# Performance work log

Hardware: AMD Instinct MI355X
Metric: run time of the kernel (lower is better)

## Reference

```python
import jax, jax.numpy as jnp
import numpy as np

RHO = 1.0
EPSILON = 0.1
N_ITERS = 5
EPS = 1e-08


def setup_inputs() -> dict:
    key = jax.random.key(0)
    k1, k2, k3 = jax.random.split(key, 3)
    B, H, M, N, D = 16, 16, 256, 576, 1024
    # student cross-attention weights: positive, rows roughly sum to 1 (post-softmax in the real model)
    sa = jax.random.uniform(k1, (B, H, M, N), dtype=jnp.float32) + 1e-3
    student_attn = sa / sa.sum(axis=-1, keepdims=True)
    visual_feats = jax.random.normal(k2, (B, N, D), dtype=jnp.float32)
    text_feats = jax.random.normal(k3, (B, M, D), dtype=jnp.float32)
    text_mask = jnp.ones((B, M), dtype=jnp.float32)
    return {"student_attn": student_attn, "visual_feats": visual_feats,
            "text_feats": text_feats, "text_mask": text_mask}


def _l2norm(x):
    return x / jnp.sqrt(jnp.sum(x * x, axis=-1, keepdims=True) + 1e-12)


def _teacher_plan(x, y, y_mask):
    # x: (B,N,D) visual, y: (B,M,D) text, y_mask: (B,M)
    B, N, D = x.shape
    M = y.shape[1]
    x_n = _l2norm(x)
    y_n = _l2norm(y)
    cost = 1.0 - jnp.einsum('bmd,bnd->bmn', y_n, x_n)          # (B,M,N)
    mu = jnp.full((B, N, 1), 1.0 / N, dtype=x.dtype)            # visual marginal (column vec)
    nu = (y_mask / (jnp.sum(y_mask, axis=1, keepdims=True) + EPS))[:, :, None]  # (B,M,1)
    K = jnp.exp(-cost / EPSILON)                                # (B,M,N)
    fi = RHO / (RHO + EPSILON)
    u = jnp.ones((B, M, 1), dtype=x.dtype)
    v = jnp.ones((B, N, 1), dtype=x.dtype)
    for _ in range(N_ITERS):
        Kv = jnp.einsum('bmn,bnk->bmk', K, v)                   # (B,M,1)
        u = (nu / (Kv + EPS)) ** fi
        Ktu = jnp.einsum('bmn,bmk->bnk', K, u)                  # (B,N,1)
        v = (mu / (Ktu + EPS)) ** fi
    P = u * K * jnp.swapaxes(v, 1, 2)                           # (B,M,N)
    return P / (jnp.sum(P, axis=-1, keepdims=True) + EPS)


def reference(student_attn, visual_feats, text_feats, text_mask):
    teacher = jax.lax.stop_gradient(_teacher_plan(visual_feats, text_feats, text_mask))
    teacher = teacher[:, None, :, :]                            # (B,1,M,N)
    loss = -jnp.sum(teacher * jnp.log(student_attn + EPS), axis=-1)  # (B,H,M)
    loss = loss * text_mask[:, None, :]
    return jnp.mean(loss)
```

## Files before the change

kernel.cpp:

```cpp
#include <hip/hip_runtime.h>
#include <math.h>

#define B_ 16
#define H_ 16
#define M_ 256
#define N_ 576
#define D_ 1024
#define BK 64
#define LDS_STRIDE (BK + 8)
#define NROWS (B_ * N_ + B_ * M_)

#define SINK_BLOCKS B_
#define SUMLOG_BLOCKS ((B_ * M_ * N_ / 4) / 1024)

constexpr float EPS_ = 1e-8f;
constexpr float FI_ = 0.90909090909090906f;

typedef __bf16 bf16x8 __attribute__((ext_vector_type(8)));
typedef float f32x4 __attribute__((ext_vector_type(4)));

__device__ __forceinline__ float wave_reduce(float v) {
#pragma unroll
  for (int o = 32; o > 0; o >>= 1) v += __shfl_down(v, o, 64);
  return v;
}

__device__ __forceinline__ unsigned short f2bf(float f) {
  union { float f; unsigned u; } a; a.f = f;
  unsigned r = a.u + 0x7fff + ((a.u >> 16) & 1);
  return (unsigned short)(r >> 16);
}

__device__ __forceinline__ float bf2f(unsigned short u) {
  union { unsigned u; float f; } a; a.u = ((unsigned)u) << 16;
  return a.f;
}

__global__ __launch_bounds__(256) void prep_kernel(const float* __restrict__ vis,
                                                   const float* __restrict__ txt,
                                                   const float* __restrict__ mask,
                                                   unsigned short* __restrict__ xb,
                                                   unsigned short* __restrict__ yb,
                                                   float* __restrict__ masksum) {
  const int bid = blockIdx.x;
  const int lane = threadIdx.x & 63;
  if (bid < NROWS / 4) {
    int wave = bid * 4 + (threadIdx.x >> 6);
    const float* src;
    unsigned short* dst;
    if (wave < B_ * N_) {
      src = vis + (size_t)wave * D_;
      dst = xb + (size_t)wave * D_;
    } else {
      int r = wave - B_ * N_;
      src = txt + (size_t)r * D_;
      dst = yb + (size_t)r * D_;
    }
    float4 v[4];
    float s = 0.f;
#pragma unroll
    for (int it = 0; it < 4; ++it) {
      v[it] = *(const float4*)&src[it * 256 + lane * 4];
      s += v[it].x * v[it].x + v[it].y * v[it].y + v[it].z * v[it].z + v[it].w * v[it].w;
    }
    s = wave_reduce(s);
    s = __shfl(s, 0, 64);
    float inv = rsqrtf(s + 1e-12f);
#pragma unroll
    for (int it = 0; it < 4; ++it) {
      ushort4 pk;
      pk.x = f2bf(v[it].x * inv);
      pk.y = f2bf(v[it].y * inv);
      pk.z = f2bf(v[it].z * inv);
      pk.w = f2bf(v[it].w * inv);
      *(ushort4*)&dst[it * 256 + lane * 4] = pk;
    }
  } else {
    int b = (bid - NROWS / 4) * 4 + (threadIdx.x >> 6);
    float4 mv = *(const float4*)&mask[b * M_ + lane * 4];
    float s = wave_reduce(mv.x + mv.y + mv.z + mv.w);
    if (lane == 0) masksum[b] = s;
  }
}

__global__ __launch_bounds__(256) void gemm_k_mfma(const unsigned short* __restrict__ xb,
                                                   const unsigned short* __restrict__ yb,
                                                   unsigned short* __restrict__ Kw) {
  __shared__ unsigned short As[64][LDS_STRIDE];
  __shared__ unsigned short Bs[64][LDS_STRIDE];
  const int b = blockIdx.z;
  const int m0 = blockIdx.y * 64;
  const int n0 = blockIdx.x * 64;
  const unsigned short* Y = yb + (size_t)b * M_ * D_;
  const unsigned short* X = xb + (size_t)b * N_ * D_;
  const int t = threadIdx.x;
  const int lane = t & 63;
  const int w = t >> 6;
  const int wm = (w & 1) * 32;
  const int wn = (w >> 1) * 32;
  const int lr = t >> 3;
  const int lc = (t & 7) * 8;
  const int fr = lane & 15;
  const int fk = (lane >> 4) * 8;

  f32x4 acc[2][2] = {};
  for (int k0 = 0; k0 < D_; k0 += BK) {
#pragma unroll
    for (int p = 0; p < 2; ++p) {
      *(uint4*)&As[lr + 32 * p][lc] = *(const uint4*)&Y[(size_t)(m0 + lr + 32 * p) * D_ + k0 + lc];
      *(uint4*)&Bs[lr + 32 * p][lc] = *(const uint4*)&X[(size_t)(n0 + lr + 32 * p) * D_ + k0 + lc];
    }
    __syncthreads();
#pragma unroll
    for (int ks = 0; ks < BK; ks += 32) {
      bf16x8 a[2], bfr[2];
#pragma unroll
      for (int i = 0; i < 2; ++i) {
        a[i] = *(const bf16x8*)&As[wm + i * 16 + fr][ks + fk];
        bfr[i] = *(const bf16x8*)&Bs[wn + i * 16 + fr][ks + fk];
      }
#pragma unroll
      for (int i = 0; i < 2; ++i)
#pragma unroll
        for (int j = 0; j < 2; ++j)
          acc[i][j] = __builtin_amdgcn_mfma_f32_16x16x32_bf16(a[i], bfr[j], acc[i][j], 0, 0, 0);
    }
    __syncthreads();
  }

  const int cm = (lane >> 4) * 4;
  const int cn = lane & 15;
#pragma unroll
  for (int i = 0; i < 2; ++i)
#pragma unroll
    for (int j = 0; j < 2; ++j)
#pragma unroll
      for (int rg = 0; rg < 4; ++rg) {
        int m = m0 + wm + i * 16 + cm + rg;
        int n = n0 + wn + j * 16 + cn;
        Kw[((size_t)b * M_ + m) * N_ + n] = f2bf(expf(10.f * (acc[i][j][rg] - 1.f)));
      }
}

__global__ __launch_bounds__(1024) void sink_sumlog_kernel(
    const unsigned short* __restrict__ Kw,
    const float* __restrict__ mask,
    const float* __restrict__ masksum,
    const float* __restrict__ student,
    float* __restrict__ SL,
    float* __restrict__ vv) {
  if (blockIdx.x >= SINK_BLOCKS) {
    const int t = threadIdx.x;
    const int idx = (blockIdx.x - SINK_BLOCKS) * 1024 + t;
    const int b = idx / (M_ * N_ / 4);
    const int cb = idx - b * (M_ * N_ / 4);
    const float* st = student + (size_t)b * H_ * M_ * N_ + (size_t)cb * 4;
    float4 acc = {0.f, 0.f, 0.f, 0.f};
#pragma unroll
    for (int h = 0; h < H_; ++h) {
      float4 s4 = *(const float4*)&st[(size_t)h * M_ * N_];
      acc.x += __logf(s4.x + EPS_);
      acc.y += __logf(s4.y + EPS_);
      acc.z += __logf(s4.z + EPS_);
      acc.w += __logf(s4.w + EPS_);
    }
    *(float4*)&SL[(size_t)b * M_ * N_ + (size_t)cb * 4] = acc;
    return;
  }

  __shared__ float u_s[M_];
  __shared__ float v_s[N_];
  __shared__ float nu_s[M_];
  __shared__ float vp[4][N_];
  const int b = blockIdx.x;
  const int t = threadIdx.x;
  const int lane = t & 63;
  const int w = t >> 6;
  const unsigned short* Kb = Kw + (size_t)b * M_ * N_;

  if (t < M_) nu_s[t] = mask[b * M_ + t] / (masksum[b] + EPS_);
  if (t < N_) v_s[t] = 1.f;
  __syncthreads();

  for (int it = 0; it < 5; ++it) {
#pragma unroll 2
    for (int r = 0; r < 16; ++r) {
      const int m = w * 16 + r;
      const unsigned short* rp = Kb + (size_t)m * N_;
      float s = 0.f;
#pragma unroll
      for (int k = 0; k < 9; ++k) s += bf2f(rp[lane + 64 * k]) * v_s[lane + 64 * k];
      s = wave_reduce(s);
      if (lane == 0) u_s[m] = powf(nu_s[m] / (s + EPS_), FI_);
    }
    __syncthreads();

    if (t < 576) {
      const int q = t / 144;
      const int c4 = (t - q * 144) * 4;
      float s0 = 0.f, s1 = 0.f, s2 = 0.f, s3 = 0.f;
#pragma unroll 8
      for (int m = q * 64; m < q * 64 + 64; ++m) {
        ushort4 k4 = *(const ushort4*)&Kb[(size_t)m * N_ + c4];
        const float um = u_s[m];
        s0 += bf2f(k4.x) * um;
        s1 += bf2f(k4.y) * um;
        s2 += bf2f(k4.z) * um;
        s3 += bf2f(k4.w) * um;
      }
      float4 r4 = {s0, s1, s2, s3};
      *(float4*)&vp[q][c4] = r4;
    }
    __syncthreads();
    if (t < N_) {
      float tot = vp[0][t] + vp[1][t] + vp[2][t] + vp[3][t];
      v_s[t] = powf((1.f / (float)N_) / (tot + EPS_), FI_);
    }
    __syncthreads();
  }
  if (t < N_) vv[b * N_ + t] = v_s[t];
}

__global__ __launch_bounds__(256) void finloss_kernel(const unsigned short* __restrict__ Kw,
                                                      const float* __restrict__ SL,
                                                      const float* __restrict__ v,
                                                      const float* __restrict__ mask,
                                                      float* __restrict__ partial) {
  __shared__ float red[2][4];
  const int m = blockIdx.x;
  const int b = blockIdx.y;
  const int t = threadIdx.x;
  float s1 = 0.f, s2 = 0.f;
  if (t < N_ / 4) {
    const unsigned short* kp = Kw + ((size_t)b * M_ + m) * N_ + t * 4;
    ushort4 k4 = *(const ushort4*)kp;
    float4 v4 = *(const float4*)&v[b * N_ + t * 4];
    float4 sl4 = *(const float4*)&SL[((size_t)b * M_ + m) * N_ + t * 4];
    float kv0 = bf2f(k4.x) * v4.x, kv1 = bf2f(k4.y) * v4.y;
    float kv2 = bf2f(k4.z) * v4.z, kv3 = bf2f(k4.w) * v4.w;
    s1 = kv0 + kv1 + kv2 + kv3;
    s2 = kv0 * sl4.x + kv1 * sl4.y + kv2 * sl4.z + kv3 * sl4.w;
  }
  s1 = wave_reduce(s1);
  s2 = wave_reduce(s2);
  if ((t & 63) == 0) { red[0][t >> 6] = s1; red[1][t >> 6] = s2; }
  __syncthreads();
  if (t == 0) {
    float S1 = red[0][0] + red[0][1] + red[0][2] + red[0][3];
    float S2 = red[1][0] + red[1][1] + red[1][2] + red[1][3];
    int row = b * M_ + m;
    partial[row] = -mask[row] * S2 / ((S1 + EPS_) * (float)(B_ * H_ * M_));
  }
}

__global__ __launch_bounds__(256) void reduce_kernel(const float* __restrict__ partial,
                                                     float* __restrict__ out) {
  __shared__ float red[4];
  float s = 0.f;
  for (int i = threadIdx.x; i < B_ * M_; i += 256) s += partial[i];
  s = wave_reduce(s);
  if ((threadIdx.x & 63) == 0) red[threadIdx.x >> 6] = s;
  __syncthreads();
  if (threadIdx.x == 0) out[0] = red[0] + red[1] + red[2] + red[3];
}

extern "C" void kernel_launch(void* const* d_in, const int* in_sizes, int n_in,
                              void* d_out, int out_size, void* d_ws, size_t ws_size,
                              hipStream_t stream) {
  const float* student = (const float*)d_in[0];
  const float* vis = (const float*)d_in[1];
  const float* txt = (const float*)d_in[2];
  const float* mask = (const float*)d_in[3];
  float* out = (float*)d_out;

  char* p = (char*)d_ws;
  unsigned short* Kb = (unsigned short*)p; p += (size_t)B_ * M_ * N_ * 2;
  unsigned short* xb = (unsigned short*)p; p += (size_t)B_ * N_ * D_ * 2;
  unsigned short* yb = (unsigned short*)p; p += (size_t)B_ * M_ * D_ * 2;
  float* SL = (float*)p;      p += (size_t)B_ * M_ * N_ * 4;
  float* vv = (float*)p;      p += B_ * N_ * 4;
  float* msum = (float*)p;    p += B_ * 4;
  float* partial = (float*)p; p += B_ * M_ * 4;

  prep_kernel<<<NROWS / 4 + 4, 256, 0, stream>>>(vis, txt, mask, xb, yb, msum);
  gemm_k_mfma<<<dim3(N_ / 64, M_ / 64, B_), 256, 0, stream>>>(xb, yb, Kb);

  sink_sumlog_kernel<<<SINK_BLOCKS + SUMLOG_BLOCKS, 1024, 0, stream>>>(
      Kb, mask, msum, student, SL, vv);

  finloss_kernel<<<dim3(M_, B_), 256, 0, stream>>>(Kb, SL, vv, mask, partial);
  reduce_kernel<<<1, 256, 0, stream>>>(partial, out);
}
```

Baseline: 399.0 us.

## Cache bf16 kernel matrix in registers across Sinkhorn iterations

Each wave loads its 16 rows of the bf16 K matrix into packed registers once, before the Sinkhorn loop. Both the row pass (K·v) and the column pass (Kᵀ·u) then run from those registers, so K is no longer re-read from global memory in each of the five iterations. The column pass now accumulates per-wave partial sums into the shared vp array in four serialized phases, separated by barriers. This raises register pressure and adds barriers in exchange for removing repeated memory traffic in a kernel that runs on only 16 blocks.

Measured after the change: 403.9 us. No clear change (+1.2%).

```diff
diff --git a/kernel.cpp b/kernel.cpp
--- a/kernel.cpp
+++ b/kernel.cpp
@@ -34,6 +34,13 @@
 __device__ __forceinline__ float bf2f(unsigned short u) {
   union { unsigned u; float f; } a; a.u = ((unsigned)u) << 16;
   return a.f;
+}
+
+__device__ __forceinline__ float bflo(unsigned p) {
+  union { unsigned u; float f; } a; a.u = p << 16; return a.f;
+}
+__device__ __forceinline__ float bfhi(unsigned p) {
+  union { unsigned u; float f; } a; a.u = p & 0xffff0000u; return a.f;
 }
 
 __global__ __launch_bounds__(256) void prep_kernel(const float* __restrict__ vis,
@@ -171,6 +178,7 @@
   __shared__ float u_s[M_];
   __shared__ float v_s[N_];
   __shared__ float nu_s[M_];
+  __shared__ float sred[M_];
   __shared__ float vp[4][N_];
   const int b = blockIdx.x;
   const int t = threadIdx.x;
@@ -178,42 +186,68 @@
   const int w = t >> 6;
   const unsigned short* Kb = Kw + (size_t)b * M_ * N_;
 
+  unsigned kp[16][4];
+  unsigned k8[8];
+#pragma unroll
+  for (int r = 0; r < 16; ++r) {
+    const unsigned short* rp = Kb + (size_t)((w << 4) + r) * N_ + lane;
+#pragma unroll
+    for (int j = 0; j < 4; ++j)
+      kp[r][j] = (unsigned)rp[128 * j] | ((unsigned)rp[128 * j + 64] << 16);
+    unsigned t8 = rp[512];
+    if (r & 1) k8[r >> 1] |= t8 << 16; else k8[r >> 1] = t8;
+  }
+
   if (t < M_) nu_s[t] = mask[b * M_ + t] / (masksum[b] + EPS_);
   if (t < N_) v_s[t] = 1.f;
   __syncthreads();
 
   for (int it = 0; it < 5; ++it) {
-#pragma unroll 2
+    float vl[9];
+#pragma unroll
+    for (int k = 0; k < 9; ++k) vl[k] = v_s[lane + 64 * k];
+
+#pragma unroll
     for (int r = 0; r < 16; ++r) {
-      const int m = w * 16 + r;
-      const unsigned short* rp = Kb + (size_t)m * N_;
       float s = 0.f;
 #pragma unroll
-      for (int k = 0; k < 9; ++k) s += bf2f(rp[lane + 64 * k]) * v_s[lane + 64 * k];
+      for (int j = 0; j < 4; ++j) {
+        s += bflo(kp[r][j]) * vl[2 * j];
+        s += bfhi(kp[r][j]) * vl[2 * j + 1];
+      }
+      s += ((r & 1) ? bfhi(k8[r >> 1]) : bflo(k8[r >> 1])) * vl[8];
       s = wave_reduce(s);
-      if (lane == 0) u_s[m] = powf(nu_s[m] / (s + EPS_), FI_);
-    }
-    __syncthreads();
-
-    if (t < 576) {
-      const int q = t / 144;
-      const int c4 = (t - q * 144) * 4;
-      float s0 = 0.f, s1 = 0.f, s2 = 0.f, s3 = 0.f;
-#pragma unroll 8
-      for (int m = q * 64; m < q * 64 + 64; ++m) {
-        ushort4 k4 = *(const ushort4*)&Kb[(size_t)m * N_ + c4];
-        const float um = u_s[m];
-        s0 += bf2f(k4.x) * um;
-        s1 += bf2f(k4.y) * um;
-        s2 += bf2f(k4.z) * um;
-        s3 += bf2f(k4.w) * um;
+      if (lane == 0) sred[(w << 4) + r] = s;
+    }
+    if (lane < 16) {
+      const int m = (w << 4) + lane;
+      u_s[m] = powf(nu_s[m] / (sred[m] + EPS_), FI_);
+    }
+
+#pragma unroll
+    for (int s = 0; s < 4; ++s) {
+      if ((w & 3) == s) {
+        const int q = w >> 2;
+        float uw[16];
+#pragma unroll
+        for (int r = 0; r < 16; ++r) uw[r] = u_s[(w << 4) + r];
+#pragma unroll
+        for (int k = 0; k < 9; ++k) {
+          float tmp = (s == 0) ? 0.f : vp[q][lane + 64 * k];
+#pragma unroll
+          for (int r = 0; r < 16; ++r) {
+            float kv;
+            if (k < 8) kv = (k & 1) ? bfhi(kp[r][k >> 1]) : bflo(kp[r][k >> 1]);
+            else       kv = (r & 1) ? bfhi(k8[r >> 1]) : bflo(k8[r >> 1]);
+            tmp += kv * uw[r];
+          }
+          vp[q][lane + 64 * k] = tmp;
+        }
       }
-      float4 r4 = {s0, s1, s2, s3};
-      *(float4*)&vp[q][c4] = r4;
-    }
-    __syncthreads();
+      __syncthreads();
+    }
     if (t < N_) {
-      float tot = vp[0][t] + vp[1][t] + vp[2][t] + vp[3][t];
+      float tot = ((vp[0][t] + vp[1][t]) + vp[2][t]) + vp[3][t];
       v_s[t] = powf((1.f / (float)N_) / (tot + EPS_), FI_);
     }
     __syncthreads();
```

## Fuse all stages into one cooperative persistent kernel with grid-wide phase syncs

Applied to the files above, without the earlier changes.

Replaces the five separate kernels with a single cooperative mega-kernel that runs prep, GEMM, ten Sinkhorn half-steps, the final loss and the reduction as phases separated by grid syncs. The Sinkhorn solve is now spread across all blocks instead of one block per batch. The student log-sum work is split into ten slices and interleaved with the Sinkhorn phases to fill idle CUs. This trades launch overhead and the serialized per-batch Sinkhorn for the cost of many grid-wide barriers and a smaller GEMM tile per block. A per-phase launch path is kept as a fallback if cooperative launch fails.

New measurement: 770.7 us. +93.2%, slower.

```diff
diff --git a/kernel.cpp b/kernel.cpp
--- a/kernel.cpp
+++ b/kernel.cpp
@@ -1,17 +1,18 @@
 #include <hip/hip_runtime.h>
+#include <hip/hip_cooperative_groups.h>
 #include <math.h>
+
+namespace cg = cooperative_groups;
 
 #define B_ 16
 #define H_ 16
 #define M_ 256
 #define N_ 576
 #define D_ 1024
-#define BK 64
-#define LDS_STRIDE (BK + 8)
 #define NROWS (B_ * N_ + B_ * M_)
-
-#define SINK_BLOCKS B_
-#define SUMLOG_BLOCKS ((B_ * M_ * N_ / 4) / 1024)
+#define SL_UNITS (B_ * M_ * N_ / 4)
+#define GEMM_TILES (B_ * (M_ / 64) * (N_ / 64))
+#define NPHASE 14
 
 constexpr float EPS_ = 1e-8f;
 constexpr float FI_ = 0.90909090909090906f;
@@ -36,232 +37,220 @@
   return a.f;
 }
 
-__global__ __launch_bounds__(256) void prep_kernel(const float* __restrict__ vis,
-                                                   const float* __restrict__ txt,
-                                                   const float* __restrict__ mask,
-                                                   unsigned short* __restrict__ xb,
-                                                   unsigned short* __restrict__ yb,
-                                                   float* __restrict__ masksum) {
+__global__ __launch_bounds__(512, 4) void mega_kernel(
+    const float* __restrict__ student, const float* __restrict__ vis,
+    const float* __restrict__ txt, const float* __restrict__ mask,
+    unsigned short* __restrict__ xb, unsigned short* __restrict__ yb,
+    unsigned short* __restrict__ Kw, float* __restrict__ SL,
+    float* __restrict__ uu, float* __restrict__ vv,
+    float* __restrict__ msum, float* __restrict__ partial,
+    float* __restrict__ out, int plo, int phi) {
+  __shared__ unsigned short As[64][72];
+  __shared__ unsigned short Bs[64][72];
+  __shared__ float part[4][64];
+  __shared__ float redf[2][2][4];
+  __shared__ float redr[4];
+
+  const int tid = threadIdx.x;
+  const int lane = tid & 63;
+  const int w = tid >> 6;
   const int bid = blockIdx.x;
-  const int lane = threadIdx.x & 63;
-  if (bid < NROWS / 4) {
-    int wave = bid * 4 + (threadIdx.x >> 6);
-    const float* src;
-    unsigned short* dst;
-    if (wave < B_ * N_) {
-      src = vis + (size_t)wave * D_;
-      dst = xb + (size_t)wave * D_;
+  const int GRID = gridDim.x;
+
+  for (int ph = plo; ph < phi; ++ph) {
+    if (ph > plo) cg::this_grid().sync();
+
+    if (ph == 0) {
+      for (int row = bid * 8 + w; row < NROWS + B_; row += GRID * 8) {
+        if (row < NROWS) {
+          const float* src;
+          unsigned short* dst;
+          if (row < B_ * N_) {
+            src = vis + (size_t)row * D_;
+            dst = xb + (size_t)row * D_;
+          } else {
+            int r = row - B_ * N_;
+            src = txt + (size_t)r * D_;
+            dst = yb + (size_t)r * D_;
+          }
+          float4 v[4];
+          float s = 0.f;
+#pragma unroll
+          for (int it = 0; it < 4; ++it) {
+            v[it] = *(const float4*)&src[it * 256 + lane * 4];
+            s += v[it].x * v[it].x + v[it].y * v[it].y + v[it].z * v[it].z + v[it].w * v[it].w;
+          }
+          s = wave_reduce(s);
+          s = __shfl(s, 0, 64);
+          float inv = rsqrtf(s + 1e-12f);
+#pragma unroll
+          for (int it = 0; it < 4; ++it) {
+            ushort4 pk;
+            pk.x = f2bf(v[it].x * inv);
+            pk.y = f2bf(v[it].y * inv);
+            pk.z = f2bf(v[it].z * inv);
+            pk.w = f2bf(v[it].w * inv);
+            *(ushort4*)&dst[it * 256 + lane * 4] = pk;
+          }
+        } else {
+          int b = row - NROWS;
+          float4 mv = *(const float4*)&mask[b * M_ + lane * 4];
+          float s = wave_reduce(mv.x + mv.y + mv.z + mv.w);
+          if (lane == 0) msum[b] = s;
+        }
+      }
+
+    } else if (ph == 1) {
+      const int lr = tid >> 3;
+      const int lc = (tid & 7) * 8;
+      const int am = (w & 3) * 16;
+      const int wn = (w >> 2) * 32;
+      const int fr = lane & 15;
+      const int fk = (lane >> 4) * 8;
+      const int cm = (lane >> 4) * 4;
+      const int cn = lane & 15;
+      for (int tt = bid; tt < GEMM_TILES; tt += GRID) {
+        const int b = tt / 36;
+        const int rem = tt - b * 36;
+        const int m0 = (rem / 9) * 64;
+        const int n0 = (rem - (rem / 9) * 9) * 64;
+        const unsigned short* Y = yb + (size_t)b * M_ * D_;
+        const unsigned short* X = xb + (size_t)b * N_ * D_;
+        f32x4 acc[2] = {};
+        for (int k0 = 0; k0 < D_; k0 += 64) {
+          __syncthreads();
+          *(uint4*)&As[lr][lc] = *(const uint4*)&Y[(size_t)(m0 + lr) * D_ + k0 + lc];
+          *(uint4*)&Bs[lr][lc] = *(const uint4*)&X[(size_t)(n0 + lr) * D_ + k0 + lc];
+          __syncthreads();
+#pragma unroll
+          for (int ks = 0; ks < 64; ks += 32) {
+            bf16x8 a = *(const bf16x8*)&As[am + fr][ks + fk];
+            bf16x8 b0 = *(const bf16x8*)&Bs[wn + fr][ks + fk];
+            bf16x8 b1 = *(const bf16x8*)&Bs[wn + 16 + fr][ks + fk];
+            acc[0] = __builtin_amdgcn_mfma_f32_16x16x32_bf16(a, b0, acc[0], 0, 0, 0);
+            acc[1] = __builtin_amdgcn_mfma_f32_16x16x32_bf16(a, b1, acc[1], 0, 0, 0);
+          }
+        }
+#pragma unroll
+        for (int j = 0; j < 2; ++j)
+#pragma unroll
+          for (int rg = 0; rg < 4; ++rg) {
+            int m = m0 + am + cm + rg;
+            int n = n0 + wn + j * 16 + cn;
+            Kw[((size_t)b * M_ + m) * N_ + n] = f2bf(expf(10.f * (acc[j][rg] - 1.f)));
+          }
+      }
+
+    } else if (ph < 12) {
+      const int sp = ph - 2;
+      if ((sp & 1) == 0) {
+        for (int row = bid * 8 + w; row < B_ * M_; row += GRID * 8) {
+          const unsigned short* rp = Kw + (size_t)row * N_;
+          float s = 0.f;
+          if (sp == 0) {
+#pragma unroll
+            for (int k = 0; k < 9; ++k) s += bf2f(rp[lane + 64 * k]);
+          } else {
+            const float* vb = vv + (row >> 8) * N_;
+#pragma unroll
+            for (int k = 0; k < 9; ++k) s += bf2f(rp[lane + 64 * k]) * vb[lane + 64 * k];
+          }
+          s = wave_reduce(s);
+          if (lane == 0) {
+            float nu = mask[row] / (msum[row >> 8] + EPS_);
+            uu[row] = powf(nu / (s + EPS_), FI_);
+          }
+        }
+      } else {
+        for (int unit = bid; unit < B_ * (N_ / 64); unit += GRID) {
+          const int b = unit / 9;
+          const int n0 = (unit - b * 9) * 64;
+          const unsigned short* Kb2 = Kw + (size_t)b * M_ * N_;
+          const float* ub = uu + b * M_;
+          if (w < 4) {
+            const int col = n0 + lane;
+            float s = 0.f;
+#pragma unroll 8
+            for (int m = w * 64; m < (w + 1) * 64; ++m)
+              s += bf2f(Kb2[(size_t)m * N_ + col]) * ub[m];
+            part[w][lane] = s;
+          }
+          __syncthreads();
+          if (tid < 64) {
+            float tot = part[0][tid] + part[1][tid] + part[2][tid] + part[3][tid];
+            vv[b * N_ + n0 + tid] = powf((1.f / (float)N_) / (tot + EPS_), FI_);
+          }
+          __syncthreads();
+        }
+      }
+      {
+        const int c0 = (int)(((long long)SL_UNITS * sp) / 10);
+        const int c1 = (int)(((long long)SL_UNITS * (sp + 1)) / 10);
+        const int nblk = (c1 - c0 + 511) >> 9;
+        const int rb = (bid + (sp * GRID) / 10) % GRID;
+        if (rb < nblk) {
+          const int u = c0 + (rb << 9) + tid;
+          if (u < c1) {
+            const int b = u / (M_ * N_ / 4);
+            const int cb = u - b * (M_ * N_ / 4);
+            const float* st = student + (size_t)b * H_ * M_ * N_ + (size_t)cb * 4;
+            float4 acc = {0.f, 0.f, 0.f, 0.f};
+#pragma unroll
+            for (int h = 0; h < H_; ++h) {
+              float4 s4 = *(const float4*)&st[(size_t)h * M_ * N_];
+              acc.x += __logf(s4.x + EPS_);
+              acc.y += __logf(s4.y + EPS_);
+              acc.z += __logf(s4.z + EPS_);
+              acc.w += __logf(s4.w + EPS_);
+            }
+            *(float4*)&SL[(size_t)b * M_ * N_ + (size_t)cb * 4] = acc;
+          }
+        }
+      }
+
+    } else if (ph == 12) {
+      const int half = tid >> 8;
+      const int lt = tid & 255;
+      const int stride = GRID * 2;
+      const int cnt = (B_ * M_ - 1 - bid * 2) / stride + 1;
+      for (int i = 0; i < cnt; ++i) {
+        const int unit = bid * 2 + half + i * stride;
+        float s1 = 0.f, s2 = 0.f;
+        if (unit < B_ * M_ && lt < 144) {
+          const int b = unit >> 8;
+          const unsigned short* kp = Kw + (size_t)unit * N_ + lt * 4;
+          ushort4 k4 = *(const ushort4*)kp;
+          float4 v4 = *(const float4*)&vv[b * N_ + lt * 4];
+          float4 sl4 = *(const float4*)&SL[(size_t)unit * N_ + lt * 4];
+          float kv0 = bf2f(k4.x) * v4.x, kv1 = bf2f(k4.y) * v4.y;
+          float kv2 = bf2f(k4.z) * v4.z, kv3 = bf2f(k4.w) * v4.w;
+          s1 = kv0 + kv1 + kv2 + kv3;
+          s2 = kv0 * sl4.x + kv1 * sl4.y + kv2 * sl4.z + kv3 * sl4.w;
+        }
+        s1 = wave_reduce(s1);
+        s2 = wave_reduce(s2);
+        if ((lt & 63) == 0) { redf[half][0][lt >> 6] = s1; redf[half][1][lt >> 6] = s2; }
+        __syncthreads();
+        if (lt == 0 && unit < B_ * M_) {
+          float S1 = redf[half][0][0] + redf[half][0][1] + redf[half][0][2] + redf[half][0][3];
+          float S2 = redf[half][1][0] + redf[half][1][1] + redf[half][1][2] + redf[half][1][3];
+          partial[unit] = -mask[unit] * S2 / ((S1 + EPS_) * (float)(B_ * H_ * M_));
+        }
+        __syncthreads();
+      }
+
     } else {
-      int r = wave - B_ * N_;
-      src = txt + (size_t)r * D_;
-      dst = yb + (size_t)r * D_;
+      if (bid == 0) {
+        float s = 0.f;
+        if (tid < 256)
+          for (int i = tid; i < B_ * M_; i += 256) s += partial[i];
+        s = wave_reduce(s);
+        if (tid < 256 && (tid & 63) == 0) redr[tid >> 6] = s;
+        __syncthreads();
+        if (tid == 0) out[0] = redr[0] + redr[1] + redr[2] + redr[3];
+      }
     }
-    float4 v[4];
-    float s = 0.f;
-#pragma unroll
-    for (int it = 0; it < 4; ++it) {
-      v[it] = *(const float4*)&src[it * 256 + lane * 4];
-      s += v[it].x * v[it].x + v[it].y * v[it].y + v[it].z * v[it].z + v[it].w * v[it].w;
-    }
-    s = wave_reduce(s);
-    s = __shfl(s, 0, 64);
-    float inv = rsqrtf(s + 1e-12f);
-#pragma unroll
-    for (int it = 0; it < 4; ++it) {
-      ushort4 pk;
-      pk.x = f2bf(v[it].x * inv);
-      pk.y = f2bf(v[it].y * inv);
-      pk.z = f2bf(v[it].z * inv);
-      pk.w = f2bf(v[it].w * inv);
-      *(ushort4*)&dst[it * 256 + lane * 4] = pk;
-    }
-  } else {
-    int b = (bid - NROWS / 4) * 4 + (threadIdx.x >> 6);
-    float4 mv = *(const float4*)&mask[b * M_ + lane * 4];
-    float s = wave_reduce(mv.x + mv.y + mv.z + mv.w);
-    if (lane == 0) masksum[b] = s;
   }
-}
-
-__global__ __launch_bounds__(256) void gemm_k_mfma(const unsigned short* __restrict__ xb,
-                                                   const unsigned short* __restrict__ yb,
-                                                   unsigned short* __restrict__ Kw) {
-  __shared__ unsigned short As[64][LDS_STRIDE];
-  __shared__ unsigned short Bs[64][LDS_STRIDE];
-  const int b = blockIdx.z;
-  const int m0 = blockIdx.y * 64;
-  const int n0 = blockIdx.x * 64;
-  const unsigned short* Y = yb + (size_t)b * M_ * D_;
-  const unsigned short* X = xb + (size_t)b * N_ * D_;
-  const int t = threadIdx.x;
-  const int lane = t & 63;
-  const int w = t >> 6;
-  const int wm = (w & 1) * 32;
-  const int wn = (w >> 1) * 32;
-  const int lr = t >> 3;
-  const int lc = (t & 7) * 8;
-  const int fr = lane & 15;
-  const int fk = (lane >> 4) * 8;
-
-  f32x4 acc[2][2] = {};
-  for (int k0 = 0; k0 < D_; k0 += BK) {
-#pragma unroll
-    for (int p = 0; p < 2; ++p) {
-      *(uint4*)&As[lr + 32 * p][lc] = *(const uint4*)&Y[(size_t)(m0 + lr + 32 * p) * D_ + k0 + lc];
-      *(uint4*)&Bs[lr + 32 * p][lc] = *(const uint4*)&X[(size_t)(n0 + lr + 32 * p) * D_ + k0 + lc];
-    }
-    __syncthreads();
-#pragma unroll
-    for (int ks = 0; ks < BK; ks += 32) {
-      bf16x8 a[2], bfr[2];
-#pragma unroll
-      for (int i = 0; i < 2; ++i) {
-        a[i] = *(const bf16x8*)&As[wm + i * 16 + fr][ks + fk];
-        bfr[i] = *(const bf16x8*)&Bs[wn + i * 16 + fr][ks + fk];
-      }
-#pragma unroll
-      for (int i = 0; i < 2; ++i)
-#pragma unroll
-        for (int j = 0; j < 2; ++j)
-          acc[i][j] = __builtin_amdgcn_mfma_f32_16x16x32_bf16(a[i], bfr[j], acc[i][j], 0, 0, 0);
-    }
-    __syncthreads();
-  }
-
-  const int cm = (lane >> 4) * 4;
-  const int cn = lane & 15;
-#pragma unroll
-  for (int i = 0; i < 2; ++i)
-#pragma unroll
-    for (int j = 0; j < 2; ++j)
-#pragma unroll
-      for (int rg = 0; rg < 4; ++rg) {
-        int m = m0 + wm + i * 16 + cm + rg;
-        int n = n0 + wn + j * 16 + cn;
-        Kw[((size_t)b * M_ + m) * N_ + n] = f2bf(expf(10.f * (acc[i][j][rg] - 1.f)));
-      }
-}
-
-__global__ __launch_bounds__(1024) void sink_sumlog_kernel(
-    const unsigned short* __restrict__ Kw,
-    const float* __restrict__ mask,
-    const float* __restrict__ masksum,
-    const float* __restrict__ student,
-    float* __restrict__ SL,
-    float* __restrict__ vv) {
-  if (blockIdx.x >= SINK_BLOCKS) {
-    const int t = threadIdx.x;
-    const int idx = (blockIdx.x - SINK_BLOCKS) * 1024 + t;
-    const int b = idx / (M_ * N_ / 4);
-    const int cb = idx - b * (M_ * N_ / 4);
-    const float* st = student + (size_t)b * H_ * M_ * N_ + (size_t)cb * 4;
-    float4 acc = {0.f, 0.f, 0.f, 0.f};
-#pragma unroll
-    for (int h = 0; h < H_; ++h) {
-      float4 s4 = *(const float4*)&st[(size_t)h * M_ * N_];
-      acc.x += __logf(s4.x + EPS_);
-      acc.y += __logf(s4.y + EPS_);
-      acc.z += __logf(s4.z + EPS_);
-      acc.w += __logf(s4.w + EPS_);
-    }
-    *(float4*)&SL[(size_t)b * M_ * N_ + (size_t)cb * 4] = acc;
-    return;
-  }
-
-  __shared__ float u_s[M_];
-  __shared__ float v_s[N_];
-  __shared__ float nu_s[M_];
-  __shared__ float vp[4][N_];
-  const int b = blockIdx.x;
-  const int t = threadIdx.x;
-  const int lane = t & 63;
-  const int w = t >> 6;
-  const unsigned short* Kb = Kw + (size_t)b * M_ * N_;
-
-  if (t < M_) nu_s[t] = mask[b * M_ + t] / (masksum[b] + EPS_);
-  if (t < N_) v_s[t] = 1.f;
-  __syncthreads();
-
-  for (int it = 0; it < 5; ++it) {
-#pragma unroll 2
-    for (int r = 0; r < 16; ++r) {
-      const int m = w * 16 + r;
-      const unsigned short* rp = Kb + (size_t)m * N_;
-      float s = 0.f;
-#pragma unroll
-      for (int k = 0; k < 9; ++k) s += bf2f(rp[lane + 64 * k]) * v_s[lane + 64 * k];
-      s = wave_reduce(s);
-      if (lane == 0) u_s[m] = powf(nu_s[m] / (s + EPS_), FI_);
-    }
-    __syncthreads();
-
-    if (t < 576) {
-      const int q = t / 144;
-      const int c4 = (t - q * 144) * 4;
-      float s0 = 0.f, s1 = 0.f, s2 = 0.f, s3 = 0.f;
-#pragma unroll 8
-      for (int m = q * 64; m < q * 64 + 64; ++m) {
-        ushort4 k4 = *(const ushort4*)&Kb[(size_t)m * N_ + c4];
-        const float um = u_s[m];
-        s0 += bf2f(k4.x) * um;
-        s1 += bf2f(k4.y) * um;
-        s2 += bf2f(k4.z) * um;
-        s3 += bf2f(k4.w) * um;
-      }
-      float4 r4 = {s0, s1, s2, s3};
-      *(float4*)&vp[q][c4] = r4;
-    }
-    __syncthreads();
-    if (t < N_) {
-      float tot = vp[0][t] + vp[1][t] + vp[2][t] + vp[3][t];
-      v_s[t] = powf((1.f / (float)N_) / (tot + EPS_), FI_);
-    }
-    __syncthreads();
-  }
-  if (t < N_) vv[b * N_ + t] = v_s[t];
-}
-
-__global__ __launch_bounds__(256) void finloss_kernel(const unsigned short* __restrict__ Kw,
-                                                      const float* __restrict__ SL,
-                                                      const float* __restrict__ v,
-                                                      const float* __restrict__ mask,
-                                                      float* __restrict__ partial) {
-  __shared__ float red[2][4];
-  const int m = blockIdx.x;
-  const int b = blockIdx.y;
-  const int t = threadIdx.x;
-  float s1 = 0.f, s2 = 0.f;
-  if (t < N_ / 4) {
-    const unsigned short* kp = Kw + ((size_t)b * M_ + m) * N_ + t * 4;
-    ushort4 k4 = *(const ushort4*)kp;
-    float4 v4 = *(const float4*)&v[b * N_ + t * 4];
-    float4 sl4 = *(const float4*)&SL[((size_t)b * M_ + m) * N_ + t * 4];
-    float kv0 = bf2f(k4.x) * v4.x, kv1 = bf2f(k4.y) * v4.y;
-    float kv2 = bf2f(k4.z) * v4.z, kv3 = bf2f(k4.w) * v4.w;
-    s1 = kv0 + kv1 + kv2 + kv3;
-    s2 = kv0 * sl4.x + kv1 * sl4.y + kv2 * sl4.z + kv3 * sl4.w;
-  }
-  s1 = wave_reduce(s1);
-  s2 = wave_reduce(s2);
-  if ((t & 63) == 0) { red[0][t >> 6] = s1; red[1][t >> 6] = s2; }
-  __syncthreads();
-  if (t == 0) {
-    float S1 = red[0][0] + red[0][1] + red[0][2] + red[0][3];
-    float S2 = red[1][0] + red[1][1] + red[1][2] + red[1][3];
-    int row = b * M_ + m;
-    partial[row] = -mask[row] * S2 / ((S1 + EPS_) * (float)(B_ * H_ * M_));
-  }
-}
-
-__global__ __launch_bounds__(256) void reduce_kernel(const float* __restrict__ partial,
-                                                     float* __restrict__ out) {
-  __shared__ float red[4];
-  float s = 0.f;
-  for (int i = threadIdx.x; i < B_ * M_; i += 256) s += partial[i];
-  s = wave_reduce(s);
-  if ((threadIdx.x & 63) == 0) red[threadIdx.x >> 6] = s;
-  __syncthreads();
-  if (threadIdx.x == 0) out[0] = red[0] + red[1] + red[2] + red[3];
 }
 
 extern "C" void kernel_launch(void* const* d_in, const int* in_sizes, int n_in,
@@ -274,20 +263,45 @@
   float* out = (float*)d_out;
 
   char* p = (char*)d_ws;
-  unsigned short* Kb = (unsigned short*)p; p += (size_t)B_ * M_ * N_ * 2;
+  unsigned short* Kw = (unsigned short*)p; p += (size_t)B_ * M_ * N_ * 2;
   unsigned short* xb = (unsigned short*)p; p += (size_t)B_ * N_ * D_ * 2;
   unsigned short* yb = (unsigned short*)p; p += (size_t)B_ * M_ * D_ * 2;
   float* SL = (float*)p;      p += (size_t)B_ * M_ * N_ * 4;
   float* vv = (float*)p;      p += B_ * N_ * 4;
+  float* uu = (float*)p;      p += B_ * M_ * 4;
   float* msum = (float*)p;    p += B_ * 4;
   float* partial = (float*)p; p += B_ * M_ * 4;
 
-  prep_kernel<<<NROWS / 4 + 4, 256, 0, stream>>>(vis, txt, mask, xb, yb, msum);
-  gemm_k_mfma<<<dim3(N_ / 64, M_ / 64, B_), 256, 0, stream>>>(xb, yb, Kb);
-
-  sink_sumlog_kernel<<<SINK_BLOCKS + SUMLOG_BLOCKS, 1024, 0, stream>>>(
-      Kb, mask, msum, student, SL, vv);
-
-  finloss_kernel<<<dim3(M_, B_), 256, 0, stream>>>(Kb, SL, vv, mask, partial);
-  reduce_kernel<<<1, 256, 0, stream>>>(partial, out);
-}
+  static int coop_blocks = -2;
+  if (coop_blocks == -2) {
+    int dev = 0;
+    (void)hipGetDevice(&dev);
+    int has_coop = 0;
+    (void)hipDeviceGetAttribute(&has_coop, hipDeviceAttributeCooperativeLaunch, dev);
+    int nb = 0;
+    hipError_t e = hipOccupancyMaxActiveBlocksPerMultiprocessor(
+        &nb, reinterpret_cast<const void*>(&mega_kernel), 512, 0);
+    coop_blocks = (has_coop && e == hipSuccess && nb >= 1) ? nb : 0;
+  }
+
+  bool launched = false;
+  if (coop_blocks > 0) {
+    int grid = coop_blocks * 256;
+    if (grid > 512) grid = 512;
+    int plo = 0, phi = NPHASE;
+    void* args[] = {(void*)&student, (void*)&vis,  (void*)&txt,  (void*)&mask,
+                    (void*)&xb,      (void*)&yb,   (void*)&Kw,   (void*)&SL,
+                    (void*)&uu,      (void*)&vv,   (void*)&msum, (void*)&partial,
+                    (void*)&out,     (void*)&plo,  (void*)&phi};
+    hipError_t e = hipLaunchCooperativeKernel(
+        reinterpret_cast<const void*>(&mega_kernel), dim3(grid), dim3(512),
+        args, 0, stream);
+    launched = (e == hipSuccess);
+  }
+  if (!launched) {
+    for (int ph2 = 0; ph2 < NPHASE; ++ph2)
+      mega_kernel<<<dim3(512), dim3(512), 0, stream>>>(
+          student, vis, txt, mask, xb, yb, Kw, SL, uu, vv, msum, partial, out,
+          ph2, ph2 + 1);
+  }
+}
```

## Split Sinkhorn across four blocks per batch with LDS slabs and fused finalization

Applied to the files above, without the earlier changes.

Moves the student log-sum pass into the GEMM launch so it runs alongside K generation. The Sinkhorn loop is split across four blocks per batch, each holding a 64-row slab of K in shared memory. Per-iteration column sums are combined through global buffers behind an atomic-counter barrier. The final loss and global reduction are folded into the same kernel with a last-block-done reduction, removing two launches. This trades the single 1024-thread block per batch and repeated global K reads for spin-wait inter-block sync, which assumes all 64 blocks are co-resident.

New measurement: 424.6 us. 1.06x slower.

```diff
diff --git a/kernel.cpp b/kernel.cpp
--- a/kernel.cpp
+++ b/kernel.cpp
@@ -9,9 +9,9 @@
 #define BK 64
 #define LDS_STRIDE (BK + 8)
 #define NROWS (B_ * N_ + B_ * M_)
-
-#define SINK_BLOCKS B_
-#define SUMLOG_BLOCKS ((B_ * M_ * N_ / 4) / 1024)
+#define SL_UNITS (B_ * M_ * N_ / 4)
+#define GEMM_BLOCKS (B_ * 4 * 9)
+#define SUMLOG_BLK (SL_UNITS / 256)
 
 constexpr float EPS_ = 1e-8f;
 constexpr float FI_ = 0.90909090909090906f;
@@ -41,7 +41,8 @@
                                                    const float* __restrict__ mask,
                                                    unsigned short* __restrict__ xb,
                                                    unsigned short* __restrict__ yb,
-                                                   float* __restrict__ masksum) {
+                                                   float* __restrict__ masksum,
+                                                   int* __restrict__ ctr) {
   const int bid = blockIdx.x;
   const int lane = threadIdx.x & 63;
   if (bid < NROWS / 4) {
@@ -76,6 +77,7 @@
       *(ushort4*)&dst[it * 256 + lane * 4] = pk;
     }
   } else {
+    if (bid == NROWS / 4 && threadIdx.x < 96) ctr[threadIdx.x] = 0;
     int b = (bid - NROWS / 4) * 4 + (threadIdx.x >> 6);
     float4 mv = *(const float4*)&mask[b * M_ + lane * 4];
     float s = wave_reduce(mv.x + mv.y + mv.z + mv.w);
@@ -83,14 +85,36 @@
   }
 }
 
-__global__ __launch_bounds__(256) void gemm_k_mfma(const unsigned short* __restrict__ xb,
-                                                   const unsigned short* __restrict__ yb,
-                                                   unsigned short* __restrict__ Kw) {
+__global__ __launch_bounds__(256) void gemm_sumlog_kernel(
+    const unsigned short* __restrict__ xb, const unsigned short* __restrict__ yb,
+    const float* __restrict__ student, unsigned short* __restrict__ Kw,
+    float* __restrict__ SL) {
   __shared__ unsigned short As[64][LDS_STRIDE];
   __shared__ unsigned short Bs[64][LDS_STRIDE];
-  const int b = blockIdx.z;
-  const int m0 = blockIdx.y * 64;
-  const int n0 = blockIdx.x * 64;
+
+  if (blockIdx.x >= GEMM_BLOCKS) {
+    const int unit = (blockIdx.x - GEMM_BLOCKS) * 256 + threadIdx.x;
+    const int b = unit / (M_ * N_ / 4);
+    const int cb = unit - b * (M_ * N_ / 4);
+    const float* st = student + (size_t)b * H_ * M_ * N_ + (size_t)cb * 4;
+    float4 acc = {0.f, 0.f, 0.f, 0.f};
+#pragma unroll
+    for (int h = 0; h < H_; ++h) {
+      float4 s4 = *(const float4*)&st[(size_t)h * M_ * N_];
+      acc.x += __logf(s4.x + EPS_);
+      acc.y += __logf(s4.y + EPS_);
+      acc.z += __logf(s4.z + EPS_);
+      acc.w += __logf(s4.w + EPS_);
+    }
+    *(float4*)&SL[(size_t)b * M_ * N_ + (size_t)cb * 4] = acc;
+    return;
+  }
+
+  const int tile = blockIdx.x;
+  const int b = tile / 36;
+  const int rem = tile - b * 36;
+  const int m0 = (rem / 9) * 64;
+  const int n0 = (rem - (rem / 9) * 9) * 64;
   const unsigned short* Y = yb + (size_t)b * M_ * D_;
   const unsigned short* X = xb + (size_t)b * N_ * D_;
   const int t = threadIdx.x;
@@ -142,126 +166,119 @@
       }
 }
 
-__global__ __launch_bounds__(1024) void sink_sumlog_kernel(
-    const unsigned short* __restrict__ Kw,
-    const float* __restrict__ mask,
-    const float* __restrict__ masksum,
-    const float* __restrict__ student,
-    float* __restrict__ SL,
-    float* __restrict__ vv) {
-  if (blockIdx.x >= SINK_BLOCKS) {
-    const int t = threadIdx.x;
-    const int idx = (blockIdx.x - SINK_BLOCKS) * 1024 + t;
-    const int b = idx / (M_ * N_ / 4);
-    const int cb = idx - b * (M_ * N_ / 4);
-    const float* st = student + (size_t)b * H_ * M_ * N_ + (size_t)cb * 4;
-    float4 acc = {0.f, 0.f, 0.f, 0.f};
-#pragma unroll
-    for (int h = 0; h < H_; ++h) {
-      float4 s4 = *(const float4*)&st[(size_t)h * M_ * N_];
-      acc.x += __logf(s4.x + EPS_);
-      acc.y += __logf(s4.y + EPS_);
-      acc.z += __logf(s4.z + EPS_);
-      acc.w += __logf(s4.w + EPS_);
-    }
-    *(float4*)&SL[(size_t)b * M_ * N_ + (size_t)cb * 4] = acc;
-    return;
-  }
-
-  __shared__ float u_s[M_];
+__global__ __launch_bounds__(256) void sink_fin_kernel(
+    const unsigned short* __restrict__ Kw, const float* __restrict__ SL,
+    const float* __restrict__ mask, const float* __restrict__ msum,
+    float* __restrict__ vp_g, int* __restrict__ ctr,
+    float* __restrict__ partial, float* __restrict__ out) {
+  __shared__ unsigned short slab[64][N_];
   __shared__ float v_s[N_];
-  __shared__ float nu_s[M_];
-  __shared__ float vp[4][N_];
-  const int b = blockIdx.x;
+  __shared__ float u_s[64];
+  __shared__ float nu_s[64];
+  __shared__ float red[2][4];
+  __shared__ float redr[4];
+  __shared__ int lastflag;
+
   const int t = threadIdx.x;
   const int lane = t & 63;
   const int w = t >> 6;
-  const unsigned short* Kb = Kw + (size_t)b * M_ * N_;
-
-  if (t < M_) nu_s[t] = mask[b * M_ + t] / (masksum[b] + EPS_);
-  if (t < N_) v_s[t] = 1.f;
+  const int b = blockIdx.x >> 2;
+  const int q = blockIdx.x & 3;
+  const int row0 = q * 64;
+
+  const unsigned short* Kbase = Kw + ((size_t)b * M_ + row0) * N_;
+  for (int i = t; i < 64 * 72; i += 256) {
+    const int r = i / 72;
+    const int c8 = (i - r * 72) * 8;
+    *(uint4*)&slab[r][c8] = *(const uint4*)&Kbase[(size_t)r * N_ + c8];
+  }
+  if (t < 64) nu_s[t] = mask[b * M_ + row0 + t] / (msum[b] + EPS_);
+  for (int n = t; n < N_; n += 256) v_s[n] = 1.f;
   __syncthreads();
+
+  float* vp_b = vp_g + (size_t)b * 2 * 4 * N_;
 
   for (int it = 0; it < 5; ++it) {
 #pragma unroll 2
     for (int r = 0; r < 16; ++r) {
       const int m = w * 16 + r;
-      const unsigned short* rp = Kb + (size_t)m * N_;
       float s = 0.f;
 #pragma unroll
-      for (int k = 0; k < 9; ++k) s += bf2f(rp[lane + 64 * k]) * v_s[lane + 64 * k];
+      for (int k = 0; k < 9; ++k) s += bf2f(slab[m][lane + 64 * k]) * v_s[lane + 64 * k];
       s = wave_reduce(s);
       if (lane == 0) u_s[m] = powf(nu_s[m] / (s + EPS_), FI_);
     }
     __syncthreads();
 
-    if (t < 576) {
-      const int q = t / 144;
-      const int c4 = (t - q * 144) * 4;
-      float s0 = 0.f, s1 = 0.f, s2 = 0.f, s3 = 0.f;
+    const int par = it & 1;
+    float* vp_out = vp_b + (size_t)(par * 4 + q) * N_;
+    for (int c = t; c < N_; c += 256) {
+      float s = 0.f;
 #pragma unroll 8
-      for (int m = q * 64; m < q * 64 + 64; ++m) {
-        ushort4 k4 = *(const ushort4*)&Kb[(size_t)m * N_ + c4];
-        const float um = u_s[m];
-        s0 += bf2f(k4.x) * um;
-        s1 += bf2f(k4.y) * um;
-        s2 += bf2f(k4.z) * um;
-        s3 += bf2f(k4.w) * um;
-      }
-      float4 r4 = {s0, s1, s2, s3};
-      *(float4*)&vp[q][c4] = r4;
-    }
-    __syncthreads();
-    if (t < N_) {
-      float tot = vp[0][t] + vp[1][t] + vp[2][t] + vp[3][t];
-      v_s[t] = powf((1.f / (float)N_) / (tot + EPS_), FI_);
-    }
-    __syncthreads();
-  }
-  if (t < N_) vv[b * N_ + t] = v_s[t];
-}
-
-__global__ __launch_bounds__(256) void finloss_kernel(const unsigned short* __restrict__ Kw,
-                                                      const float* __restrict__ SL,
-                                                      const float* __restrict__ v,
-                                                      const float* __restrict__ mask,
-                                                      float* __restrict__ partial) {
-  __shared__ float red[2][4];
-  const int m = blockIdx.x;
-  const int b = blockIdx.y;
-  const int t = threadIdx.x;
-  float s1 = 0.f, s2 = 0.f;
-  if (t < N_ / 4) {
-    const unsigned short* kp = Kw + ((size_t)b * M_ + m) * N_ + t * 4;
-    ushort4 k4 = *(const ushort4*)kp;
-    float4 v4 = *(const float4*)&v[b * N_ + t * 4];
-    float4 sl4 = *(const float4*)&SL[((size_t)b * M_ + m) * N_ + t * 4];
-    float kv0 = bf2f(k4.x) * v4.x, kv1 = bf2f(k4.y) * v4.y;
-    float kv2 = bf2f(k4.z) * v4.z, kv3 = bf2f(k4.w) * v4.w;
-    s1 = kv0 + kv1 + kv2 + kv3;
-    s2 = kv0 * sl4.x + kv1 * sl4.y + kv2 * sl4.z + kv3 * sl4.w;
-  }
-  s1 = wave_reduce(s1);
-  s2 = wave_reduce(s2);
-  if ((t & 63) == 0) { red[0][t >> 6] = s1; red[1][t >> 6] = s2; }
+      for (int m = 0; m < 64; ++m) s += bf2f(slab[m][c]) * u_s[m];
+      vp_out[c] = s;
+    }
+    __syncthreads();
+
+    if (t == 0) {
+      __threadfence();
+      __hip_atomic_fetch_add(&ctr[b * 5 + it], 1, __ATOMIC_RELEASE,
+                             __HIP_MEMORY_SCOPE_AGENT);
+      while (__hip_atomic_load(&ctr[b * 5 + it], __ATOMIC_ACQUIRE,
+                               __HIP_MEMORY_SCOPE_AGENT) < 4)
+        __builtin_amdgcn_s_sleep(1);
+    }
+    __syncthreads();
+    __threadfence();
+
+    const float* vp0 = vp_b + (size_t)par * 4 * N_;
+    for (int n = t; n < N_; n += 256) {
+      float tot = ((vp0[n] + vp0[N_ + n]) + vp0[2 * N_ + n]) + vp0[3 * N_ + n];
+      v_s[n] = powf((1.f / (float)N_) / (tot + EPS_), FI_);
+    }
+    __syncthreads();
+  }
+
+  for (int r = 0; r < 64; ++r) {
+    const int row = b * M_ + row0 + r;
+    float s1 = 0.f, s2 = 0.f;
+    if (t < 144) {
+      ushort4 k4 = *(const ushort4*)&slab[r][t * 4];
+      float4 v4 = *(const float4*)&v_s[t * 4];
+      float4 sl4 = *(const float4*)&SL[(size_t)row * N_ + t * 4];
+      float kv0 = bf2f(k4.x) * v4.x, kv1 = bf2f(k4.y) * v4.y;
+      float kv2 = bf2f(k4.z) * v4.z, kv3 = bf2f(k4.w) * v4.w;
+      s1 = kv0 + kv1 + kv2 + kv3;
+      s2 = kv0 * sl4.x + kv1 * sl4.y + kv2 * sl4.z + kv3 * sl4.w;
+    }
+    s1 = wave_reduce(s1);
+    s2 = wave_reduce(s2);
+    if ((t & 63) == 0) { red[0][t >> 6] = s1; red[1][t >> 6] = s2; }
+    __syncthreads();
+    if (t == 0) {
+      float S1 = red[0][0] + red[0][1] + red[0][2] + red[0][3];
+      float S2 = red[1][0] + red[1][1] + red[1][2] + red[1][3];
+      partial[row] = -mask[row] * S2 / ((S1 + EPS_) * (float)(B_ * H_ * M_));
+    }
+    __syncthreads();
+  }
+
+  if (t == 0) {
+    __threadfence();
+    int fin = __hip_atomic_fetch_add(&ctr[80], 1, __ATOMIC_ACQ_REL,
+                                     __HIP_MEMORY_SCOPE_AGENT);
+    lastflag = (fin == 63);
+  }
   __syncthreads();
-  if (t == 0) {
-    float S1 = red[0][0] + red[0][1] + red[0][2] + red[0][3];
-    float S2 = red[1][0] + red[1][1] + red[1][2] + red[1][3];
-    int row = b * M_ + m;
-    partial[row] = -mask[row] * S2 / ((S1 + EPS_) * (float)(B_ * H_ * M_));
-  }
-}
-
-__global__ __launch_bounds__(256) void reduce_kernel(const float* __restrict__ partial,
-                                                     float* __restrict__ out) {
-  __shared__ float red[4];
-  float s = 0.f;
-  for (int i = threadIdx.x; i < B_ * M_; i += 256) s += partial[i];
-  s = wave_reduce(s);
-  if ((threadIdx.x & 63) == 0) red[threadIdx.x >> 6] = s;
-  __syncthreads();
-  if (threadIdx.x == 0) out[0] = red[0] + red[1] + red[2] + red[3];
+  if (lastflag) {
+    __threadfence();
+    float s = 0.f;
+    for (int i = t; i < B_ * M_; i += 256) s += partial[i];
+    s = wave_reduce(s);
+    if ((t & 63) == 0) redr[t >> 6] = s;
+    __syncthreads();
+    if (t == 0) out[0] = redr[0] + redr[1] + redr[2] + redr[3];
+  }
 }
 
 extern "C" void kernel_launch(void* const* d_in, const int* in_sizes, int n_in,
@@ -274,20 +291,16 @@
   float* out = (float*)d_out;
 
   char* p = (char*)d_ws;
-  unsigned short* Kb = (unsigned short*)p; p += (size_t)B_ * M_ * N_ * 2;
+  unsigned short* Kw = (unsigned short*)p; p += (size_t)B_ * M_ * N_ * 2;
   unsigned short* xb = (unsigned short*)p; p += (size_t)B_ * N_ * D_ * 2;
   unsigned short* yb = (unsigned short*)p; p += (size_t)B_ * M_ * D_ * 2;
   float* SL = (float*)p;      p += (size_t)B_ * M_ * N_ * 4;
-  float* vv = (float*)p;      p += B_ * N_ * 4;
-  float* msum = (float*)p;    p += B_ * 4;
-  float* partial = (float*)p; p += B_ * M_ * 4;
-
-  prep_kernel<<<NROWS / 4 + 4, 256, 0, stream>>>(vis, txt, mask, xb, yb, msum);
-  gemm_k_mfma<<<dim3(N_ / 64, M_ / 64, B_), 256, 0, stream>>>(xb, yb, Kb);
-
-  sink_sumlog_kernel<<<SINK_BLOCKS + SUMLOG_BLOCKS, 1024, 0, stream>>>(
-      Kb, mask, msum, student, SL, vv);
-
-  finloss_kernel<<<dim3(M_, B_), 256, 0, stream>>>(Kb, SL, vv, mask, partial);
-  reduce_kernel<<<1, 256, 0, stream>>>(partial, out);
-}
+  float* msum = (float*)p;    p += 256;
+  float* partial = (float*)p; p += (size_t)B_ * M_ * 4;
+  float* vp_g = (float*)p;    p += (size_t)B_ * 2 * 4 * N_ * 4;
+  int* ctr = (int*)p;         p += 96 * 4;
+
+  prep_kernel<<<NROWS / 4 + 4, 256, 0, stream>>>(vis, txt, mask, xb, yb, msum, ctr);
+  gemm_sumlog_kernel<<<GEMM_BLOCKS + SUMLOG_BLK, 256, 0, stream>>>(xb, yb, student, Kw, SL);
+  sink_fin_kernel<<<B_ * 4, 256, 0, stream>>>(Kw, SL, mask, msum, vp_g, ctr, partial, out);
+}
```
